# Optimization experiments

Measured on AMD Instinct MI355X. Metric: run time of the kernel, lower is better.

## Reference

```python
import jax, jax.numpy as jnp
import numpy as np

B, S, H, NH = 8, 1024, 1024, 16
HD = H // NH


def setup_inputs() -> dict:
    key = jax.random.key(0)
    ks = jax.random.split(key, 9)
    scale = 0.02
    d = {"x": jax.random.normal(ks[0], (B, S, H), jnp.float32)}
    for i, n in enumerate(["q", "k", "v", "o"]):
        d["W" + n] = jax.random.normal(ks[1 + i], (H, H), jnp.float32) * scale
        d["b" + n] = jnp.zeros((H,), jnp.float32)
    d["position_idx"] = jnp.arange(S, dtype=jnp.int32).reshape(1, S)
    return d


def _rotate_half(x):
    x1, x2 = jnp.split(x, 2, axis=-1)
    return jnp.concatenate([-x2, x1], axis=-1)


def _apply_rope(x, position_idx):
    # Faithful to source (precedence bug included): (10000**arange) / head_dim
    inv_freq = 1.0 / (10000.0 ** jnp.arange(0, HD, 2, dtype=jnp.float32) / HD)
    freqs = jnp.einsum('bi,j->bij', position_idx.astype(jnp.float32), inv_freq)  # [1,S,HD/2]
    emb = jnp.concatenate([freqs, freqs], axis=-1)  # [1,S,HD]
    cos = jnp.cos(emb).reshape(1, 1, -1, HD)
    sin = jnp.sin(emb).reshape(1, 1, -1, HD)
    return x * cos + _rotate_half(x) * sin


def reference(x, Wq, bq, Wk, bk, Wv, bv, Wo, bo, position_idx):
    b, s, _ = x.shape

    def to_heads(t):  # [b,s,H] -> [b,nh,s,hd]
        return t.reshape(b, s, NH, HD).transpose(0, 2, 1, 3)

    q = to_heads(x @ Wq + bq)
    k = to_heads(x @ Wk + bk)
    v = to_heads(x @ Wv + bv)
    q = _apply_rope(q, position_idx)
    k = _apply_rope(k, position_idx)
    scores = jnp.einsum('bhqd,bhkd->bhqk', q, k) / jnp.sqrt(jnp.float32(HD))
    attn = jax.nn.softmax(scores, axis=-1)
    out = jnp.einsum('bhqk,bhkd->bhqd', attn, v)  # [b,nh,s,hd]
    out = out.transpose(0, 2, 1, 3).reshape(b, s, NH * HD)
    return out @ Wo + bo
```

## Files before the change

kernel.cpp:

```cpp
#include <hip/hip_runtime.h>
#include <hip/hip_bf16.h>
#include <math.h>

#define B_  8
#define S_  1024
#define H_  1024
#define NH_ 16
#define HD_ 64
#define M_  (B_*S_)
#define K_  1024

typedef __hip_bfloat16 bf16;
typedef __attribute__((ext_vector_type(8))) short  short8;
typedef __attribute__((ext_vector_type(4))) short  short4v;
typedef __attribute__((ext_vector_type(8))) __bf16 bf16x8;
typedef __attribute__((ext_vector_type(4))) float  f32x4;

#define MFMA16(a, b, c) __builtin_amdgcn_mfma_f32_16x16x32_bf16((a), (b), (c), 0, 0, 0)
#define QSCALE 0.18033688011112042f

static __device__ __forceinline__ short f2bf_s(float f) {
  unsigned u = __float_as_uint(f);
  u += 0x7fffu + ((u >> 16) & 1u);
  return (short)(u >> 16);
}
static __device__ __forceinline__ float bf2f_s(short s) {
  return __uint_as_float((unsigned)(unsigned short)s << 16);
}

static __device__ __forceinline__ void gload16(const void* g, void* l) {
  __builtin_amdgcn_global_load_lds(
      (const __attribute__((address_space(1))) void*)g,
      (__attribute__((address_space(3))) void*)l, 16, 0, 0);
}

__global__ __launch_bounds__(256) void convert_x_kernel(const float* __restrict__ x,
                                                        short* __restrict__ xb) {
  int i = blockIdx.x * 256 + threadIdx.x;
  size_t base = (size_t)i * 8;
  f32x4 a = *(const f32x4*)(x + base);
  f32x4 b = *(const f32x4*)(x + base + 4);
  short8 v;
  #pragma unroll
  for (int j = 0; j < 4; ++j) { v[j] = f2bf_s(a[j]); v[4 + j] = f2bf_s(b[j]); }
  *(short8*)(xb + base) = v;
}

__global__ void ingest_bias_kernel(const float* __restrict__ b0, const float* __restrict__ b1,
                                   const float* __restrict__ b2, const float* __restrict__ b3,
                                   short* __restrict__ bbuf) {
  int i = blockIdx.x * 256 + threadIdx.x;
  if (i >= 4096) return;
  const float* src = (i < 1024) ? b0 : (i < 2048) ? b1 : (i < 3072) ? b2 : b3;
  bbuf[i] = f2bf_s(src[i & 1023]);
}

__global__ void rope_tables_kernel(const int* __restrict__ pos,
                                   float* __restrict__ cost, float* __restrict__ sint) {
  int i = blockIdx.x * blockDim.x + threadIdx.x;
  if (i >= S_ * 32) return;
  int s = i >> 5, f = i & 31;
  double inv = 64.0 / pow(10000.0, (double)(2 * f));
  double ang = (double)pos[s] * inv;
  cost[i] = (float)cos(ang);
  sint[i] = (float)sin(ang);
}

__global__ __launch_bounds__(256) void transpose_w_kernel(
    const float* __restrict__ w0, const float* __restrict__ w1,
    const float* __restrict__ w2, const float* __restrict__ w3,
    bf16* __restrict__ outbase) {
  const float* src = (blockIdx.y == 0) ? w0 : (blockIdx.y == 1) ? w1 : (blockIdx.y == 2) ? w2 : w3;
  short* dst = (short*)outbase + (size_t)blockIdx.y * H_ * H_;
  __shared__ short tile[64][72];
  const int t = threadIdx.x;
  const int tr = blockIdx.x >> 4, tc = blockIdx.x & 15;
  const int r0 = tr * 64, c0 = tc * 64;
  #pragma unroll
  for (int p = 0; p < 2; ++p) {
    int row = p * 32 + (t >> 3);
    int c8  = (t & 7) * 8;
    const float* f = src + (size_t)(r0 + row) * H_ + c0 + c8;
    #pragma unroll
    for (int j = 0; j < 8; ++j) tile[c8 + j][row] = f2bf_s(f[j]);
  }
  __syncthreads();
  #pragma unroll
  for (int p = 0; p < 2; ++p) {
    int row = p * 32 + (t >> 3);
    int c8  = (t & 7) * 8;
    short8 v;
    #pragma unroll
    for (int j = 0; j < 8; ++j) v[j] = tile[row][c8 + j];
    *(short8*)(dst + (size_t)(c0 + row) * H_ + r0 + c8) = v;
  }
}

__global__ __launch_bounds__(256) void gemm_bt_kernel(
    const bf16* __restrict__ A, const bf16* __restrict__ Bt, const short* __restrict__ bias,
    void* __restrict__ C, void* __restrict__ C2, void* __restrict__ C3,
    const float* __restrict__ cost, const float* __restrict__ sint,
    int mode, float qscale) {
  __shared__ short sA[128 * 32];
  __shared__ short sB[128 * 32];
  const int t  = threadIdx.x;
  const int bm = blockIdx.y * 128, bn = blockIdx.x * 128;
  const int lane = t & 63, wid = t >> 6;
  const int wr = wid >> 1, wc = wid & 1;
  const int lm = lane & 15, lg = lane >> 4;
  f32x4 acc[4][4] = {};

  const short* Ag = (const short*)A;
  const short* Bg = (const short*)Bt;

  for (int k0 = 0; k0 < K_; k0 += 32) {
    #pragma unroll
    for (int c = 0; c < 2; ++c) {
      int flat = c * 256 + t;
      int row = flat >> 2, k8 = (flat & 3) * 8;
      gload16(Ag + (size_t)(bm + row) * K_ + k0 + k8, sA + flat * 8);
      gload16(Bg + (size_t)(bn + row) * K_ + k0 + k8, sB + flat * 8);
    }
    __syncthreads();
    bf16x8 af[4], bfr[4];
    #pragma unroll
    for (int i = 0; i < 4; ++i) af[i]  = *(const bf16x8*)(sA + (wr * 64 + i * 16 + lm) * 32 + lg * 8);
    #pragma unroll
    for (int j = 0; j < 4; ++j) bfr[j] = *(const bf16x8*)(sB + (wc * 64 + j * 16 + lm) * 32 + lg * 8);
    #pragma unroll
    for (int i = 0; i < 4; ++i)
      #pragma unroll
      for (int j = 0; j < 4; ++j)
        acc[i][j] = MFMA16(af[i], bfr[j], acc[i][j]);
    __syncthreads();
  }

  if (mode == 0) {
    #pragma unroll
    for (int i = 0; i < 4; ++i) {
      int row = bm + wr * 64 + i * 16 + lg * 4;
      #pragma unroll
      for (int j = 0; j < 4; ++j) {
        int col = bn + wc * 64 + j * 16 + lm;
        float bv = bf2f_s(bias[col]);
        #pragma unroll
        for (int r = 0; r < 4; ++r)
          ((float*)C)[(size_t)(row + r) * H_ + col] = acc[i][j][r] + bv;
      }
    }
  } else {
    int region = bn >> 10;
    if (region < 2) {
      short* dst = (short*)(region ? C2 : C);
      float qs = region ? 1.0f : qscale;
      #pragma unroll
      for (int i = 0; i < 4; ++i) {
        int row = bm + wr * 64 + i * 16 + lg * 4;
        #pragma unroll
        for (int j = 0; j < 2; ++j) {
          int col0 = bn + wc * 64 + j * 16 + lm;
          int d = col0 & 63;
          int dcol = col0 & 1023;
          float b0 = bf2f_s(bias[col0]);
          float b1 = bf2f_s(bias[col0 + 32]);
          #pragma unroll
          for (int r = 0; r < 4; ++r) {
            int s = (row + r) & (S_ - 1);
            float cv = cost[s * 32 + d] * qs, sv = sint[s * 32 + d] * qs;
            float x1 = acc[i][j][r] + b0;
            float x2 = acc[i][j + 2][r] + b1;
            dst[(size_t)(row + r) * H_ + dcol]      = f2bf_s(x1 * cv - x2 * sv);
            dst[(size_t)(row + r) * H_ + dcol + 32] = f2bf_s(x2 * cv + x1 * sv);
          }
        }
      }
    } else {
      #pragma unroll
      for (int i = 0; i < 4; ++i) {
        int row = bm + wr * 64 + i * 16 + lg * 4;
        int bb = row >> 10;
        int sb = row & 1023;
        int pos = (sb & ~31) | (((sb >> 2) & 3) << 3) | (((sb >> 4) & 1) << 2);
        #pragma unroll
        for (int j = 0; j < 4; ++j) {
          int col = bn + wc * 64 + j * 16 + lm;
          int colv = col & 1023;
          float bv = bf2f_s(bias[col]);
          short4v pk;
          #pragma unroll
          for (int r = 0; r < 4; ++r) pk[r] = f2bf_s(acc[i][j][r] + bv);
          short* dstp = (short*)C3 + ((size_t)(bb * NH_ + (colv >> 6)) * HD_ + (colv & 63)) * S_ + pos;
          *(short4v*)dstp = pk;
        }
      }
    }
  }
}

__global__ __launch_bounds__(256) void attn_kernel(
    const bf16* __restrict__ q, const bf16* __restrict__ k,
    const bf16* __restrict__ vt, bf16* __restrict__ o) {
  const int bh = blockIdx.x, b = bh >> 4, h = bh & 15;
  const int t = threadIdx.x, wid = t >> 6, lane = t & 63;
  const int lm = lane & 15, lg = lane >> 4;
  const int qw = blockIdx.y * 128 + wid * 32;

  __shared__ short sK[32 * 64];
  __shared__ short sV[64 * 32];

  const int keyr = t >> 3, ccK = t & 7, tcK = ccK ^ (keyr & 7);
  const int dr   = t >> 2, ccV = t & 3, tcV = ccV ^ (dr & 3);
  const short* ksrc = (const short*)k + (size_t)(b * S_ + keyr) * H_ + h * HD_ + tcK * 8;
  const short* vsrc = (const short*)vt + (size_t)bh * HD_ * S_ + (size_t)dr * S_ + tcV * 8;
  short* kdst = sK + t * 8;
  short* vdst = sV + t * 8;

  const int kO0 = lm * 64 + ((lg ^ (lm & 7)) << 3);
  const int kO1 = lm * 64 + (((4 + lg) ^ (lm & 7)) << 3);
  const int vO  = lm * 32 + ((lg ^ (lm & 3)) << 3);

  const short* qbase = (const short*)q + (size_t)(b * S_ + qw) * H_ + h * HD_;
  bf16x8 qf[2][2];
  #pragma unroll
  for (int mi = 0; mi < 2; ++mi)
    #pragma unroll
    for (int dh = 0; dh < 2; ++dh)
      qf[mi][dh] = *(const bf16x8*)(qbase + (size_t)(mi * 16 + lm) * H_ + dh * 32 + lg * 8);

  float ps[2] = {0.f, 0.f};
  f32x4 oacc[2][4] = {};

  for (int kk = 0; kk < S_; kk += 32) {
    gload16(ksrc + (size_t)kk * H_, kdst);
    gload16(vsrc + kk, vdst);
    __syncthreads();

    f32x4 sc[2][2] = {};
    #pragma unroll
    for (int nt = 0; nt < 2; ++nt) {
      bf16x8 kf0 = *(const bf16x8*)(sK + nt * 16 * 64 + kO0);
      bf16x8 kf1 = *(const bf16x8*)(sK + nt * 16 * 64 + kO1);
      #pragma unroll
      for (int mi = 0; mi < 2; ++mi) {
        sc[mi][nt] = MFMA16(kf0, qf[mi][0], sc[mi][nt]);
        sc[mi][nt] = MFMA16(kf1, qf[mi][1], sc[mi][nt]);
      }
    }
    bf16x8 vf[4];
    #pragma unroll
    for (int dt = 0; dt < 4; ++dt)
      vf[dt] = *(const bf16x8*)(sV + dt * 16 * 32 + vO);

    bf16x8 pf[2];
    #pragma unroll
    for (int mi = 0; mi < 2; ++mi)
      #pragma unroll
      for (int nt = 0; nt < 2; ++nt)
        #pragma unroll
        for (int r = 0; r < 4; ++r) {
          float p = exp2f(fminf(sc[mi][nt][r], 115.0f));
          ps[mi] += p;
          pf[mi][nt * 4 + r] = (__bf16)p;
        }
    #pragma unroll
    for (int mi = 0; mi < 2; ++mi)
      #pragma unroll
      for (int dt = 0; dt < 4; ++dt)
        oacc[mi][dt] = MFMA16(pf[mi], vf[dt], oacc[mi][dt]);
    __syncthreads();
  }
  #pragma unroll
  for (int mi = 0; mi < 2; ++mi) {
    ps[mi] += __shfl_xor(ps[mi], 16);
    ps[mi] += __shfl_xor(ps[mi], 32);
  }
  #pragma unroll
  for (int mi = 0; mi < 2; ++mi) {
    #pragma unroll
    for (int r = 0; r < 4; ++r) {
      float rr = 1.0f / __shfl(ps[mi], lg * 4 + r);
      int row = qw + mi * 16 + lg * 4 + r;
      #pragma unroll
      for (int dt = 0; dt < 4; ++dt) {
        int col = h * HD_ + dt * 16 + lm;
        ((short*)o)[(size_t)(b * S_ + row) * H_ + col] = f2bf_s(oacc[mi][dt][r] * rr);
      }
    }
  }
}

extern "C" void kernel_launch(void* const* d_in, const int* in_sizes, int n_in,
                              void* d_out, int out_size, void* d_ws, size_t ws_size,
                              hipStream_t stream) {
  (void)out_size; (void)ws_size;
  int ix, iWq, iWk, iWv, iWo, ibq, ibk, ibv, ibo, ipos;
  const int XS = 8388608, WS = 1048576;
  if (n_in == 10 && in_sizes[0] == WS && in_sizes[9] == XS) {
    iWk = 0; iWo = 1; iWq = 2; iWv = 3; ibk = 4; ibo = 5; ibq = 6; ibv = 7; ipos = 8; ix = 9;
  } else if (n_in == 10 && in_sizes[0] == 1024 && in_sizes[9] == XS) {
    ipos = 0; ibo = 1; iWo = 2; ibv = 3; iWv = 4; ibk = 5; iWk = 6; ibq = 7; iWq = 8; ix = 9;
  } else if (n_in == 10 && in_sizes[0] == XS && in_sizes[1] == 1024) {
    ix = 0; ipos = 1; ibv = 2; ibq = 3; ibo = 4; ibk = 5; iWv = 6; iWq = 7; iWo = 8; iWk = 9;
  } else {
    ix = 0; iWq = 1; ibq = 2; iWk = 3; ibk = 4; iWv = 5; ibv = 6; iWo = 7; ibo = 8; ipos = 9;
  }
  const float* x  = (const float*)d_in[ix];
  const float* Wq = (const float*)d_in[iWq];
  const float* bq = (const float*)d_in[ibq];
  const float* Wk = (const float*)d_in[iWk];
  const float* bk = (const float*)d_in[ibk];
  const float* Wv = (const float*)d_in[iWv];
  const float* bv = (const float*)d_in[ibv];
  const float* Wo = (const float*)d_in[iWo];
  const float* bo = (const float*)d_in[ibo];
  const int*  pos = (const int*)d_in[ipos];

  char* ws = (char*)d_ws;
  bf16* wt    = (bf16*)(ws);
  bf16* kb    = (bf16*)(ws + (8ull  << 20));
  bf16* vtb   = (bf16*)(ws + (24ull << 20));
  bf16* obuf  = (bf16*)(ws + (40ull << 20));
  float* cost = (float*)(ws + (40ull << 20));
  float* sint = (float*)(ws + (40ull << 20) + (size_t)S_ * 32 * sizeof(float));
  short* bbuf = (short*)(ws + (56ull << 20));
  bf16* qb    = (bf16*)d_out;
  short* xb   = (short*)((char*)d_out + (16ull << 20));

  const int NEL = H_ * H_;
  rope_tables_kernel<<<dim3(128), 256, 0, stream>>>(pos, cost, sint);
  ingest_bias_kernel<<<dim3(16), 256, 0, stream>>>(bq, bk, bv, bo, bbuf);
  transpose_w_kernel<<<dim3(256, 4), 256, 0, stream>>>(Wq, Wk, Wv, Wo, wt);
  convert_x_kernel<<<dim3(4096), 256, 0, stream>>>(x, xb);
  gemm_bt_kernel<<<dim3(24, 64), 256, 0, stream>>>((const bf16*)xb, wt, bbuf,
                                                   qb, kb, vtb, cost, sint, 3, QSCALE);
  attn_kernel<<<dim3(128, 8), 256, 0, stream>>>(qb, kb, vtb, obuf);
  gemm_bt_kernel<<<dim3(8, 64), 256, 0, stream>>>(obuf, wt + 3 * NEL, bbuf + 3072,
                                                  d_out, nullptr, nullptr, cost, sint, 0, 1.0f);
}
```

Baseline: 202.8 us.

## Split fused QKV GEMM into three launches and double-buffer attention K/V tiles

The single fused QKV projection launch (24x64 grid) becomes three separate 8x64 launches, one each for Q, K and V, with mode-specific epilogues. The attention kernel now double-buffers its K/V shared-memory tiles, prefetching the next key block while computing on the current one, and drops one barrier per iteration. Splitting the GEMM adds launch overhead and smaller grids, while double buffering doubles attention LDS use to overlap global loads with MFMA work.

```diff
diff --git a/kernel.cpp b/kernel.cpp
--- a/kernel.cpp
+++ b/kernel.cpp
@@ -98,8 +98,7 @@
 
 __global__ __launch_bounds__(256) void gemm_bt_kernel(
     const bf16* __restrict__ A, const bf16* __restrict__ Bt, const short* __restrict__ bias,
-    void* __restrict__ C, void* __restrict__ C2, void* __restrict__ C3,
-    const float* __restrict__ cost, const float* __restrict__ sint,
+    void* __restrict__ C, const float* __restrict__ cost, const float* __restrict__ sint,
     int mode, float qscale) {
   __shared__ short sA[128 * 32];
   __shared__ short sB[128 * 32];
@@ -148,50 +147,44 @@
           ((float*)C)[(size_t)(row + r) * H_ + col] = acc[i][j][r] + bv;
       }
     }
+  } else if (mode == 1) {
+    #pragma unroll
+    for (int i = 0; i < 4; ++i) {
+      int row = bm + wr * 64 + i * 16 + lg * 4;
+      #pragma unroll
+      for (int j = 0; j < 2; ++j) {
+        int col0 = bn + wc * 64 + j * 16 + lm;
+        int d = col0 & 63;
+        float b0 = bf2f_s(bias[col0]);
+        float b1 = bf2f_s(bias[col0 + 32]);
+        #pragma unroll
+        for (int r = 0; r < 4; ++r) {
+          int s = (row + r) & (S_ - 1);
+          float cv = cost[s * 32 + d] * qscale, sv = sint[s * 32 + d] * qscale;
+          float x1 = acc[i][j][r] + b0;
+          float x2 = acc[i][j + 2][r] + b1;
+          ((short*)C)[(size_t)(row + r) * H_ + col0]      = f2bf_s(x1 * cv - x2 * sv);
+          ((short*)C)[(size_t)(row + r) * H_ + col0 + 32] = f2bf_s(x2 * cv + x1 * sv);
+        }
+      }
+    }
   } else {
-    int region = bn >> 10;
-    if (region < 2) {
-      short* dst = (short*)(region ? C2 : C);
-      float qs = region ? 1.0f : qscale;
-      #pragma unroll
-      for (int i = 0; i < 4; ++i) {
-        int row = bm + wr * 64 + i * 16 + lg * 4;
+    #pragma unroll
+    for (int i = 0; i < 4; ++i) {
+      int row = bm + wr * 64 + i * 16 + lg * 4;
+      int bb = row >> 10;
+      int sb = row & 1023;
+      int pos = (sb & ~31) | (((sb >> 2) & 3) << 3) | (((sb >> 4) & 1) << 2);
+      #pragma unroll
+      for (int j = 0; j < 4; ++j) {
+        int col = bn + wc * 64 + j * 16 + lm;
+        int colv = col & 1023;
+        float bv = bf2f_s(bias[col]);
+        short4v pk;
         #pragma unroll
-        for (int j = 0; j < 2; ++j) {
-          int col0 = bn + wc * 64 + j * 16 + lm;
-          int d = col0 & 63;
-          int dcol = col0 & 1023;
-          float b0 = bf2f_s(bias[col0]);
-          float b1 = bf2f_s(bias[col0 + 32]);
-          #pragma unroll
-          for (int r = 0; r < 4; ++r) {
-            int s = (row + r) & (S_ - 1);
-            float cv = cost[s * 32 + d] * qs, sv = sint[s * 32 + d] * qs;
-            float x1 = acc[i][j][r] + b0;
-            float x2 = acc[i][j + 2][r] + b1;
-            dst[(size_t)(row + r) * H_ + dcol]      = f2bf_s(x1 * cv - x2 * sv);
-            dst[(size_t)(row + r) * H_ + dcol + 32] = f2bf_s(x2 * cv + x1 * sv);
-          }
-        }
-      }
-    } else {
-      #pragma unroll
-      for (int i = 0; i < 4; ++i) {
-        int row = bm + wr * 64 + i * 16 + lg * 4;
-        int bb = row >> 10;
-        int sb = row & 1023;
-        int pos = (sb & ~31) | (((sb >> 2) & 3) << 3) | (((sb >> 4) & 1) << 2);
-        #pragma unroll
-        for (int j = 0; j < 4; ++j) {
-          int col = bn + wc * 64 + j * 16 + lm;
-          int colv = col & 1023;
-          float bv = bf2f_s(bias[col]);
-          short4v pk;
-          #pragma unroll
-          for (int r = 0; r < 4; ++r) pk[r] = f2bf_s(acc[i][j][r] + bv);
-          short* dstp = (short*)C3 + ((size_t)(bb * NH_ + (colv >> 6)) * HD_ + (colv & 63)) * S_ + pos;
-          *(short4v*)dstp = pk;
-        }
+        for (int r = 0; r < 4; ++r) pk[r] = f2bf_s(acc[i][j][r] + bv);
+        short* dstp = (short*)C + ((size_t)(bb * NH_ + (colv >> 6)) * HD_ + (colv & 63)) * S_ + pos;
+        *(short4v*)dstp = pk;
       }
     }
   }
@@ -205,15 +198,13 @@
   const int lm = lane & 15, lg = lane >> 4;
   const int qw = blockIdx.y * 128 + wid * 32;
 
-  __shared__ short sK[32 * 64];
-  __shared__ short sV[64 * 32];
+  __shared__ short sK[2][32 * 64];
+  __shared__ short sV[2][64 * 32];
 
   const int keyr = t >> 3, ccK = t & 7, tcK = ccK ^ (keyr & 7);
   const int dr   = t >> 2, ccV = t & 3, tcV = ccV ^ (dr & 3);
   const short* ksrc = (const short*)k + (size_t)(b * S_ + keyr) * H_ + h * HD_ + tcK * 8;
   const short* vsrc = (const short*)vt + (size_t)bh * HD_ * S_ + (size_t)dr * S_ + tcV * 8;
-  short* kdst = sK + t * 8;
-  short* vdst = sV + t * 8;
 
   const int kO0 = lm * 64 + ((lg ^ (lm & 7)) << 3);
   const int kO1 = lm * 64 + (((4 + lg) ^ (lm & 7)) << 3);
@@ -230,16 +221,24 @@
   float ps[2] = {0.f, 0.f};
   f32x4 oacc[2][4] = {};
 
+  gload16(ksrc, sK[0] + t * 8);
+  gload16(vsrc, sV[0] + t * 8);
+  __syncthreads();
+
+  int cur = 0;
   for (int kk = 0; kk < S_; kk += 32) {
-    gload16(ksrc + (size_t)kk * H_, kdst);
-    gload16(vsrc + kk, vdst);
-    __syncthreads();
+    if (kk + 32 < S_) {
+      gload16(ksrc + (size_t)(kk + 32) * H_, sK[cur ^ 1] + t * 8);
+      gload16(vsrc + (kk + 32), sV[cur ^ 1] + t * 8);
+    }
+    const short* sKc = sK[cur];
+    const short* sVc = sV[cur];
 
     f32x4 sc[2][2] = {};
     #pragma unroll
     for (int nt = 0; nt < 2; ++nt) {
-      bf16x8 kf0 = *(const bf16x8*)(sK + nt * 16 * 64 + kO0);
-      bf16x8 kf1 = *(const bf16x8*)(sK + nt * 16 * 64 + kO1);
+      bf16x8 kf0 = *(const bf16x8*)(sKc + nt * 16 * 64 + kO0);
+      bf16x8 kf1 = *(const bf16x8*)(sKc + nt * 16 * 64 + kO1);
       #pragma unroll
       for (int mi = 0; mi < 2; ++mi) {
         sc[mi][nt] = MFMA16(kf0, qf[mi][0], sc[mi][nt]);
@@ -249,7 +248,7 @@
     bf16x8 vf[4];
     #pragma unroll
     for (int dt = 0; dt < 4; ++dt)
-      vf[dt] = *(const bf16x8*)(sV + dt * 16 * 32 + vO);
+      vf[dt] = *(const bf16x8*)(sVc + dt * 16 * 32 + vO);
 
     bf16x8 pf[2];
     #pragma unroll
@@ -267,7 +266,9 @@
       #pragma unroll
       for (int dt = 0; dt < 4; ++dt)
         oacc[mi][dt] = MFMA16(pf[mi], vf[dt], oacc[mi][dt]);
+
     __syncthreads();
+    cur ^= 1;
   }
   #pragma unroll
   for (int mi = 0; mi < 2; ++mi) {
@@ -331,9 +332,13 @@
   ingest_bias_kernel<<<dim3(16), 256, 0, stream>>>(bq, bk, bv, bo, bbuf);
   transpose_w_kernel<<<dim3(256, 4), 256, 0, stream>>>(Wq, Wk, Wv, Wo, wt);
   convert_x_kernel<<<dim3(4096), 256, 0, stream>>>(x, xb);
-  gemm_bt_kernel<<<dim3(24, 64), 256, 0, stream>>>((const bf16*)xb, wt, bbuf,
-                                                   qb, kb, vtb, cost, sint, 3, QSCALE);
+  gemm_bt_kernel<<<dim3(8, 64), 256, 0, stream>>>((const bf16*)xb, wt + 0 * NEL, bbuf + 0,
+                                                  qb,  cost, sint, 1, QSCALE);
+  gemm_bt_kernel<<<dim3(8, 64), 256, 0, stream>>>((const bf16*)xb, wt + 1 * NEL, bbuf + 1024,
+                                                  kb,  cost, sint, 1, 1.0f);
+  gemm_bt_kernel<<<dim3(8, 64), 256, 0, stream>>>((const bf16*)xb, wt + 2 * NEL, bbuf + 2048,
+                                                  vtb, cost, sint, 2, 1.0f);
   attn_kernel<<<dim3(128, 8), 256, 0, stream>>>(qb, kb, vtb, obuf);
   gemm_bt_kernel<<<dim3(8, 64), 256, 0, stream>>>(obuf, wt + 3 * NEL, bbuf + 3072,
-                                                  d_out, nullptr, nullptr, cost, sint, 0, 1.0f);
-}
+                                                  d_out, cost, sint, 0, 1.0f);
+}
```

Result: no change. 202.1 us (-0.3%).
